# Optimization experiments

Measured on AMD Instinct MI355X. Metric: run time of the kernel, lower is better.

The kernel has to match this reference:

```python
import math
import jax, jax.numpy as jnp
import numpy as np

B, S, H = 4, 2048, 1024

def setup_inputs() -> dict:
    key = jax.random.key(0)
    k1, k2, k3, k4 = jax.random.split(key, 4)
    X = jax.random.normal(k1, (B, S, H), dtype=jnp.float32)
    attention_mask = jax.random.randint(k2, (B, S), 0, 2).astype(jnp.bool_)
    W = jax.random.normal(k3, (H, 3 * H), dtype=jnp.float32) * (1.0 / math.sqrt(H))
    b = jax.random.normal(k4, (3 * H,), dtype=jnp.float32) * 0.02
    return {"X": X, "attention_mask": attention_mask, "W": W, "b": b}

def reference(X, attention_mask, W, b):
    hidden_dim = X.shape[-1]
    # fused QKV projection: (B,S,3H)
    QKV = X @ W + b
    Q, K, V = jnp.split(QKV, 3, axis=-1)
    # scores: (B, S, S)
    scores = jnp.einsum('bqd,bkd->bqk', Q, K) / math.sqrt(hidden_dim)
    # 2D key-padding mask (B,S) -> broadcast over query dim; True = masked
    mask = attention_mask[:, None, :]  # (B,1,S) broadcasts to (B,S,S)
    scores = jnp.where(mask, -jnp.inf, scores)
    attn = jax.nn.softmax(scores, axis=-1)
    # dropout_rate = 0.0 (eval): identity
    return jnp.einsum('bqk,bkd->bqd', attn, V)
```

## Files before the change

### kernel.cpp

```cpp
#include <hip/hip_runtime.h>
#include <hip/hip_bf16.h>
#include <stdint.h>


typedef __attribute__((ext_vector_type(8))) short bf16x8;
typedef __attribute__((ext_vector_type(4))) float f32x4;

__device__ __forceinline__ void async_cp16(const void* g, void* l) {
  __builtin_amdgcn_global_load_lds(
      (const __attribute__((address_space(1))) void*)g,
      (__attribute__((address_space(3))) void*)l, 16, 0, 0);
}

__device__ __forceinline__ uint32_t laddr(const void* p) {
  return (uint32_t)(uintptr_t)(const __attribute__((address_space(3))) void*)p;
}

#define FENCE() asm volatile("" ::: "memory")
#define BAR()                           \
  do {                                  \
    FENCE();                            \
    __builtin_amdgcn_s_barrier();       \
    FENCE();                            \
  } while (0)
#define VMW(N) asm volatile("s_waitcnt vmcnt(" #N ")" ::: "memory")
#define LGKM0()                                            \
  do {                                                     \
    asm volatile("s_waitcnt lgkmcnt(0)" ::: "memory");     \
    __builtin_amdgcn_sched_barrier(0);                     \
  } while (0)
#define DSR(dst, a, OFF) \
  asm volatile("ds_read_b128 %0, %1 offset:" #OFF : "=v"(dst) : "v"(a))

__global__ __launch_bounds__(256) void prep(
    const float* __restrict__ X, __hip_bfloat16* __restrict__ Xb,
    const float* __restrict__ W, __hip_bfloat16* __restrict__ Wt,
    const int* __restrict__ mask, int* __restrict__ idx,
    int* __restrict__ cnt, int* __restrict__ cnt_pad,
    float* __restrict__ rowsum) {
  const int b = blockIdx.x;
  const int tid = threadIdx.x;
  if (b < 8192) {
    int i = (b * 256 + tid) * 4;
    float4 f = *(const float4*)(X + i);
    __hip_bfloat16 o[4];
    o[0] = __float2bfloat16(f.x);
    o[1] = __float2bfloat16(f.y);
    o[2] = __float2bfloat16(f.z);
    o[3] = __float2bfloat16(f.w);
    *(ushort4*)(Xb + i) = *(const ushort4*)o;
    return;
  }
  if (b < 11264) {
    __shared__ float tile[32][33];
    const int t = b - 8192;
    const int bx = (t % 96) * 32;
    const int by = (t / 96) * 32;
    const int tx = tid & 31, ty = tid >> 5;
#pragma unroll
    for (int j = 0; j < 4; ++j)
      tile[ty + j * 8][tx] = W[(int64_t)(by + ty + j * 8) * 3072 + bx + tx];
    __syncthreads();
#pragma unroll
    for (int j = 0; j < 4; ++j)
      Wt[(int64_t)(bx + ty + j * 8) * 1024 + by + tx] =
          __float2bfloat16(tile[tx][ty + j * 8]);
    return;
  }
  {
    const int z = b - 11264;
    const int* mz = mask + z * 2048;
    int* iz = idx + z * 2048;
    const int lane = tid & 63, wave = tid >> 6;
    float* rs = rowsum + z * 2048;
#pragma unroll
    for (int j = 0; j < 8; ++j) rs[tid + j * 256] = 0.f;

    int keep[8];
    int local = 0;
#pragma unroll
    for (int j = 0; j < 8; ++j) {
      keep[j] = (mz[tid * 8 + j] == 0);
      local += keep[j];
    }
    int pre = local;
#pragma unroll
    for (int off = 1; off <= 32; off <<= 1) {
      int n = __shfl_up(pre, off, 64);
      if (lane >= off) pre += n;
    }
    __shared__ int wsum[4];
    if (lane == 63) wsum[wave] = pre;
    __syncthreads();
    int base = 0;
    for (int w = 0; w < wave; ++w) base += wsum[w];
    int excl = base + pre - local;
#pragma unroll
    for (int j = 0; j < 8; ++j)
      if (keep[j]) iz[excl++] = tid * 8 + j;
    if (tid == 255) {
      int tot = base + pre;
      cnt[z] = tot;
      cnt_pad[z] = (tot + 127) & ~127;
    }
  }
}

__global__ __launch_bounds__(256) void gemm_qkv(
    const __hip_bfloat16* __restrict__ Xb, const __hip_bfloat16* __restrict__ Wt,
    const float* __restrict__ bias, const int* __restrict__ idx,
    const int* __restrict__ cnt, const int* __restrict__ cnt_pad,
    __hip_bfloat16* __restrict__ Q, __hip_bfloat16* __restrict__ Kc,
    __hip_bfloat16* __restrict__ Vt) {
  const int z = blockIdx.z;
  const int f = blockIdx.x;
  const int xcd = f & 7, loc = f >> 3;
  const int m0 = ((loc & 7) * 2 + (xcd >> 2)) * 128;
  const int n_idx = (loc >> 3) * 4 + (xcd & 3);
  const bool isQ = (n_idx < 8);
  if (!isQ && m0 >= cnt_pad[z]) return;
  const int n0 = (isQ ? n_idx : n_idx - 8) * 128;
  const __hip_bfloat16* A = Xb + (int64_t)z * 2048 * 1024;
  const __hip_bfloat16* Bt = Wt + (isQ ? 0 : (int64_t)1024 * 1024);
  const float* bv = bias + (isQ ? 0 : 1024);

  const int tid = threadIdx.x;
  const int wave = tid >> 6, lane = tid & 63;
  const int quad = lane >> 4, tr = lane & 15, t7 = tr & 7;
  const int wm = wave & 1, wn = wave >> 1;

  __shared__ __hip_bfloat16 ls[32768];

  const __hip_bfloat16* gsrc[8];
  int loff[8];
  {
    const int srow = lane >> 3;
    const int kcs = (((lane & 7) ^ srow) * 8);
    const int cz = isQ ? 0 : cnt[z];
    const int* idxz = idx + z * 2048;
#pragma unroll
    for (int cc = 0; cc < 8; ++cc) {
      int c = wave * 8 + cc;
      int isA = (c < 16);
      int cr = isA ? c : (c - 16);
      int row = cr * 8 + srow;
      if (isA) {
        int ar = m0 + row;
        if (!isQ) ar = (ar < cz) ? idxz[ar] : 0;
        gsrc[cc] = A + (int64_t)ar * 1024 + kcs;
      } else {
        gsrc[cc] = Bt + (int64_t)(n0 + row) * 1024 + kcs;
      }
      loff[cc] = (isA ? 0 : 8192) + cr * 512;
    }
  }

  uint32_t aAd[2][2], bBd[2][2];
  {
    uint32_t base = laddr(ls);
#pragma unroll
    for (int b = 0; b < 2; ++b)
#pragma unroll
      for (int w = 0; w < 2; ++w) {
        uint32_t col = (uint32_t)(((((w << 2) | quad)) ^ t7) * 16);
        aAd[b][w] = base + b * 32768 + (wm * 64 + tr) * 128 + col;
        bBd[b][w] = base + b * 32768 + 16384 + (wn * 64 + tr) * 128 + col;
      }
  }

  f32x4 acc[4][4];
#pragma unroll
  for (int mi = 0; mi < 4; ++mi)
#pragma unroll
    for (int ni = 0; ni < 4; ++ni) acc[mi][ni] = (f32x4){0.f, 0.f, 0.f, 0.f};

  bf16x8 af[4], bf[4];

#define STAGE(BUF, k0)                                            \
  do {                                                            \
    _Pragma("unroll") for (int cc = 0; cc < 8; ++cc)              \
        async_cp16(gsrc[cc] + (k0), ls + (BUF)*16384 + loff[cc]); \
  } while (0)
#define COMP(BUF)                                                             \
  do {                                                                        \
    _Pragma("unroll") for (int w = 0; w < 2; ++w) {                           \
      DSR(af[0], aAd[BUF][w], 0);                                             \
      DSR(af[1], aAd[BUF][w], 2048);                                          \
      DSR(af[2], aAd[BUF][w], 4096);                                          \
      DSR(af[3], aAd[BUF][w], 6144);                                          \
      DSR(bf[0], bBd[BUF][w], 0);                                             \
      DSR(bf[1], bBd[BUF][w], 2048);                                          \
      DSR(bf[2], bBd[BUF][w], 4096);                                          \
      DSR(bf[3], bBd[BUF][w], 6144);                                          \
      LGKM0();                                                                \
      _Pragma("unroll") for (int mi = 0; mi < 4; ++mi)                        \
          _Pragma("unroll") for (int ni = 0; ni < 4; ++ni) acc[mi][ni] =      \
              __builtin_amdgcn_mfma_f32_16x16x32_bf16(af[mi], bf[ni],         \
                                                      acc[mi][ni], 0, 0, 0);  \
    }                                                                         \
  } while (0)

  STAGE(0, 0);
  for (int it = 0; it < 8; ++it) {
    STAGE(1, (2 * it + 1) * 64);
    VMW(8); BAR();
    COMP(0);
    BAR();
    if (it < 7) {
      STAGE(0, (2 * it + 2) * 64);
      VMW(8);
    } else {
      VMW(0);
    }
    BAR();
    COMP(1);
    BAR();
  }
#undef STAGE
#undef COMP

  const int rowbase = m0 + wm * 64;
  const int colbase = n0 + wn * 64;
  if (isQ) {
    __hip_bfloat16* C = Q + (int64_t)z * 2048 * 1024;
#pragma unroll
    for (int ni = 0; ni < 4; ++ni) {
      int col = colbase + ni * 16 + tr;
      float bb = bv[col];
#pragma unroll
      for (int mi = 0; mi < 4; ++mi) {
        int row = rowbase + mi * 16 + quad * 4;
#pragma unroll
        for (int r = 0; r < 4; ++r)
          C[(int64_t)(row + r) * 1024 + col] =
              __float2bfloat16(acc[mi][ni][r] + bb);
      }
    }
  } else if (n0 < 1024) {
    __hip_bfloat16* C = Kc + (int64_t)z * 2048 * 1024;
#pragma unroll
    for (int ni = 0; ni < 4; ++ni) {
      int col = colbase + ni * 16 + tr;
      float bb = bv[col];
#pragma unroll
      for (int mi = 0; mi < 4; ++mi) {
        int row = rowbase + mi * 16 + quad * 4;
#pragma unroll
        for (int r = 0; r < 4; ++r)
          C[(int64_t)(row + r) * 1024 + col] =
              __float2bfloat16(acc[mi][ni][r] + bb);
      }
    }
  } else {
    __syncthreads();
#pragma unroll
    for (int ni = 0; ni < 4; ++ni) {
      int cl = wn * 64 + ni * 16 + tr;
      float bb = bv[colbase + ni * 16 + tr];
#pragma unroll
      for (int mi = 0; mi < 4; ++mi) {
        int rl = wm * 64 + mi * 16 + quad * 4;
        __hip_bfloat16 h[4];
#pragma unroll
        for (int r = 0; r < 4; ++r) h[r] = __float2bfloat16(acc[mi][ni][r] + bb);
        *(ushort4*)(ls + cl * 136 + rl) = *(const ushort4*)h;
      }
    }
    __syncthreads();
    __hip_bfloat16* Vz = Vt + (int64_t)z * 1024 * 2048;
    const int d0 = n0 - 1024;
    const int seg = tid & 15;
#pragma unroll
    for (int p = 0; p < 8; ++p) {
      int d = p * 16 + (tid >> 4);
      bf16x8 v = *(const bf16x8*)(ls + d * 136 + seg * 8);
      *(bf16x8*)(Vz + (int64_t)(d0 + d) * 2048 + m0 + seg * 8) = v;
    }
  }
}

__global__ __launch_bounds__(256) void gemm_scores(
    const __hip_bfloat16* __restrict__ Qb, const __hip_bfloat16* __restrict__ Kc,
    __hip_bfloat16* __restrict__ Sc, float* __restrict__ rowsum,
    const int* __restrict__ cnt, const int* __restrict__ cnt_pad,
    float scale2) {
  const int z = blockIdx.z;
  const int f = blockIdx.x;
  const int xcd = f & 7, loc = f >> 3;
  const int m0 = ((loc & 7) * 2 + (xcd >> 2)) * 128;
  const int n0 = ((loc >> 3) * 4 + (xcd & 3)) * 128;
  if (n0 >= cnt_pad[z]) return;
  const __hip_bfloat16* A = Qb + (int64_t)z * 2048 * 1024;
  const __hip_bfloat16* Bt = Kc + (int64_t)z * 2048 * 1024;

  const int tid = threadIdx.x;
  const int wave = tid >> 6, lane = tid & 63;
  const int quad = lane >> 4, tr = lane & 15, t7 = tr & 7;
  const int wm = wave & 1, wn = wave >> 1;

  __shared__ __hip_bfloat16 ls[32768];

  const __hip_bfloat16* gsrc[8];
  int loff[8];
  {
    const int srow = lane >> 3;
    const int kcs = (((lane & 7) ^ srow) * 8);
#pragma unroll
    for (int cc = 0; cc < 8; ++cc) {
      int c = wave * 8 + cc;
      int isA = (c < 16);
      int cr = isA ? c : (c - 16);
      int row = cr * 8 + srow;
      gsrc[cc] = isA ? (A + (int64_t)(m0 + row) * 1024 + kcs)
                     : (Bt + (int64_t)(n0 + row) * 1024 + kcs);
      loff[cc] = (isA ? 0 : 8192) + cr * 512;
    }
  }

  uint32_t aAd[2][2], bBd[2][2];
  {
    uint32_t base = laddr(ls);
#pragma unroll
    for (int b = 0; b < 2; ++b)
#pragma unroll
      for (int w = 0; w < 2; ++w) {
        uint32_t col = (uint32_t)(((((w << 2) | quad)) ^ t7) * 16);
        aAd[b][w] = base + b * 32768 + (wm * 64 + tr) * 128 + col;
        bBd[b][w] = base + b * 32768 + 16384 + (wn * 64 + tr) * 128 + col;
      }
  }

  f32x4 acc[4][4];
#pragma unroll
  for (int mi = 0; mi < 4; ++mi)
#pragma unroll
    for (int ni = 0; ni < 4; ++ni) acc[mi][ni] = (f32x4){0.f, 0.f, 0.f, 0.f};

  bf16x8 af[4], bf[4];

#define STAGE(BUF, k0)                                            \
  do {                                                            \
    _Pragma("unroll") for (int cc = 0; cc < 8; ++cc)              \
        async_cp16(gsrc[cc] + (k0), ls + (BUF)*16384 + loff[cc]); \
  } while (0)
#define COMP(BUF)                                                             \
  do {                                                                        \
    _Pragma("unroll") for (int w = 0; w < 2; ++w) {                           \
      DSR(af[0], aAd[BUF][w], 0);                                             \
      DSR(af[1], aAd[BUF][w], 2048);                                          \
      DSR(af[2], aAd[BUF][w], 4096);                                          \
      DSR(af[3], aAd[BUF][w], 6144);                                          \
      DSR(bf[0], bBd[BUF][w], 0);                                             \
      DSR(bf[1], bBd[BUF][w], 2048);                                          \
      DSR(bf[2], bBd[BUF][w], 4096);                                          \
      DSR(bf[3], bBd[BUF][w], 6144);                                          \
      LGKM0();                                                                \
      _Pragma("unroll") for (int mi = 0; mi < 4; ++mi)                        \
          _Pragma("unroll") for (int ni = 0; ni < 4; ++ni) acc[mi][ni] =      \
              __builtin_amdgcn_mfma_f32_16x16x32_bf16(af[mi], bf[ni],         \
                                                      acc[mi][ni], 0, 0, 0);  \
    }                                                                         \
  } while (0)

  STAGE(0, 0);
  for (int it = 0; it < 8; ++it) {
    STAGE(1, (2 * it + 1) * 64);
    VMW(8); BAR();
    COMP(0);
    BAR();
    if (it < 7) {
      STAGE(0, (2 * it + 2) * 64);
      VMW(8);
    } else {
      VMW(0);
    }
    BAR();
    COMP(1);
    BAR();
  }
#undef STAGE
#undef COMP

  const int rowbase = m0 + wm * 64;
  const int colbase = n0 + wn * 64;
  const int cn = cnt[z];
  __hip_bfloat16* C = Sc + (int64_t)z * 2048 * 2048;

  float psum[4][4];
#pragma unroll
  for (int mi = 0; mi < 4; ++mi)
#pragma unroll
    for (int r = 0; r < 4; ++r) psum[mi][r] = 0.f;

#pragma unroll
  for (int ni = 0; ni < 4; ++ni) {
    int col = colbase + ni * 16 + tr;
    bool valid = (col < cn);
#pragma unroll
    for (int mi = 0; mi < 4; ++mi) {
      int row = rowbase + mi * 16 + quad * 4;
#pragma unroll
      for (int r = 0; r < 4; ++r) {
        float e = valid ? exp2f(acc[mi][ni][r] * scale2) : 0.f;
        C[(int64_t)(row + r) * 2048 + col] = __float2bfloat16(e);
        psum[mi][r] += e;
      }
    }
  }
#pragma unroll
  for (int off = 1; off <= 8; off <<= 1)
#pragma unroll
    for (int mi = 0; mi < 4; ++mi)
#pragma unroll
      for (int r = 0; r < 4; ++r)
        psum[mi][r] += __shfl_xor(psum[mi][r], off, 64);
  if (tr == 0) {
    float* rs = rowsum + z * 2048 + rowbase;
#pragma unroll
    for (int mi = 0; mi < 4; ++mi)
#pragma unroll
      for (int r = 0; r < 4; ++r)
        atomicAdd(&rs[mi * 16 + quad * 4 + r], psum[mi][r]);
  }
}

__global__ __launch_bounds__(256) void gemm_pv(
    const __hip_bfloat16* __restrict__ Sc, const __hip_bfloat16* __restrict__ Vt,
    float* __restrict__ out, const float* __restrict__ rowsum,
    const int* __restrict__ cnt_pad) {
  const int z = blockIdx.z;
  const int f = blockIdx.x;
  const int xcd = f & 7, loc = f >> 3;
  const int m0 = ((loc & 7) * 2 + (xcd >> 2)) * 128;
  const int n0 = ((loc >> 3) * 4 + (xcd & 3)) * 128;
  const int Ks = cnt_pad[z];
  const __hip_bfloat16* A = Sc + (int64_t)z * 2048 * 2048;
  const __hip_bfloat16* Bt = Vt + (int64_t)z * 1024 * 2048;

  const int tid = threadIdx.x;
  const int wave = tid >> 6, lane = tid & 63;
  const int quad = lane >> 4, tr = lane & 15, t7 = tr & 7;
  const int wm = wave & 1, wn = wave >> 1;

  __shared__ __hip_bfloat16 ls[32768];

  const __hip_bfloat16* gsrc[8];
  int loff[8];
  {
    const int srow = lane >> 3;
    const int kcs = (((lane & 7) ^ srow) * 8);
#pragma unroll
    for (int cc = 0; cc < 8; ++cc) {
      int c = wave * 8 + cc;
      int isA = (c < 16);
      int cr = isA ? c : (c - 16);
      int row = cr * 8 + srow;
      gsrc[cc] = isA ? (A + (int64_t)(m0 + row) * 2048 + kcs)
                     : (Bt + (int64_t)(n0 + row) * 2048 + kcs);
      loff[cc] = (isA ? 0 : 8192) + cr * 512;
    }
  }

  uint32_t aAd[2][2], bBd[2][2];
  {
    uint32_t base = laddr(ls);
#pragma unroll
    for (int b = 0; b < 2; ++b)
#pragma unroll
      for (int w = 0; w < 2; ++w) {
        uint32_t col = (uint32_t)(((((w << 2) | quad)) ^ t7) * 16);
        aAd[b][w] = base + b * 32768 + (wm * 64 + tr) * 128 + col;
        bBd[b][w] = base + b * 32768 + 16384 + (wn * 64 + tr) * 128 + col;
      }
  }

  f32x4 acc[4][4];
#pragma unroll
  for (int mi = 0; mi < 4; ++mi)
#pragma unroll
    for (int ni = 0; ni < 4; ++ni) acc[mi][ni] = (f32x4){0.f, 0.f, 0.f, 0.f};

  bf16x8 af[4], bf[4];

#define STAGE(BUF, k0)                                            \
  do {                                                            \
    _Pragma("unroll") for (int cc = 0; cc < 8; ++cc)              \
        async_cp16(gsrc[cc] + (k0), ls + (BUF)*16384 + loff[cc]); \
  } while (0)
#define COMP(BUF)                                                             \
  do {                                                                        \
    _Pragma("unroll") for (int w = 0; w < 2; ++w) {                           \
      DSR(af[0], aAd[BUF][w], 0);                                             \
      DSR(af[1], aAd[BUF][w], 2048);                                          \
      DSR(af[2], aAd[BUF][w], 4096);                                          \
      DSR(af[3], aAd[BUF][w], 6144);                                          \
      DSR(bf[0], bBd[BUF][w], 0);                                             \
      DSR(bf[1], bBd[BUF][w], 2048);                                          \
      DSR(bf[2], bBd[BUF][w], 4096);                                          \
      DSR(bf[3], bBd[BUF][w], 6144);                                          \
      LGKM0();                                                                \
      _Pragma("unroll") for (int mi = 0; mi < 4; ++mi)                        \
          _Pragma("unroll") for (int ni = 0; ni < 4; ++ni) acc[mi][ni] =      \
              __builtin_amdgcn_mfma_f32_16x16x32_bf16(af[mi], bf[ni],         \
                                                      acc[mi][ni], 0, 0, 0);  \
    }                                                                         \
  } while (0)

  const int NP = Ks >> 7;
  STAGE(0, 0);
  for (int it = 0; it < NP; ++it) {
    STAGE(1, (2 * it + 1) * 64);
    VMW(8); BAR();
    COMP(0);
    BAR();
    if (it + 1 < NP) {
      STAGE(0, (2 * it + 2) * 64);
      VMW(8);
    } else {
      VMW(0);
    }
    BAR();
    COMP(1);
    BAR();
  }
#undef STAGE
#undef COMP

  const int rowbase = m0 + wm * 64;
  const int colbase = n0 + wn * 64;
  const float* rs = rowsum + z * 2048 + rowbase;
  float invv[4][4];
#pragma unroll
  for (int mi = 0; mi < 4; ++mi)
#pragma unroll
    for (int r = 0; r < 4; ++r) invv[mi][r] = 1.0f / rs[mi * 16 + quad * 4 + r];

  float* C = out + (int64_t)z * 2048 * 1024;
#pragma unroll
  for (int ni = 0; ni < 4; ++ni) {
    int col = colbase + ni * 16 + tr;
#pragma unroll
    for (int mi = 0; mi < 4; ++mi) {
      int row = rowbase + mi * 16 + quad * 4;
#pragma unroll
      for (int r = 0; r < 4; ++r)
        C[(int64_t)(row + r) * 1024 + col] = acc[mi][ni][r] * invv[mi][r];
    }
  }
}

extern "C" void kernel_launch(void* const* d_in, const int* in_sizes, int n_in,
                              void* d_out, int out_size, void* d_ws,
                              size_t ws_size, hipStream_t stream) {
  const float* X = (const float*)d_in[0];
  const int* mask = (const int*)d_in[1];
  const float* W = (const float*)d_in[2];
  const float* bias = (const float*)d_in[3];
  float* out = (float*)d_out;

  char* ws = (char*)d_ws;
  auto alloc = [&](size_t bytes) {
    char* p = ws;
    ws += (bytes + 255) & ~(size_t)255;
    return p;
  };
  __hip_bfloat16* Xb = (__hip_bfloat16*)alloc(8192ULL * 1024 * 2);
  __hip_bfloat16* Wt = (__hip_bfloat16*)alloc(3072ULL * 1024 * 2);
  __hip_bfloat16* Q = (__hip_bfloat16*)alloc(8192ULL * 1024 * 2);
  __hip_bfloat16* Kc = (__hip_bfloat16*)alloc(4ULL * 2048 * 1024 * 2);
  __hip_bfloat16* Vt = (__hip_bfloat16*)alloc(4ULL * 1024 * 2048 * 2);
  __hip_bfloat16* Sc = (__hip_bfloat16*)alloc(4ULL * 2048 * 2048 * 2);
  float* rowsum = (float*)alloc(8192ULL * 4);
  int* idx = (int*)alloc(4ULL * 2048 * 4);
  int* cnt = (int*)alloc(64);
  int* cnt_pad = (int*)alloc(64);

  prep<<<11268, 256, 0, stream>>>(X, Xb, W, Wt, mask, idx, cnt, cnt_pad,
                                  rowsum);
  gemm_qkv<<<dim3(384, 1, 4), 256, 0, stream>>>(Xb, Wt, bias, idx, cnt,
                                                cnt_pad, Q, Kc, Vt);
  gemm_scores<<<dim3(256, 1, 4), 256, 0, stream>>>(
      Q, Kc, Sc, rowsum, cnt, cnt_pad, 0.03125f * 1.4426950408889634f);
  gemm_pv<<<dim3(128, 1, 4), 256, 0, stream>>>(Sc, Vt, out, rowsum, cnt_pad);
}
```

Before: 191.7 us.

## Fuse QKV, scores and PV GEMMs into one persistent kernel with dependency counters

Replaces three separate GEMM launches with a single persistent kernel of 512 blocks. Blocks pull tiles from an atomic work queue, and later stages spin-wait on per-tile completion counters instead of relying on kernel boundaries. The goal is to remove launch gaps and the tail idling at each stage boundary, so that scores and PV tiles can start while earlier stages finish. In exchange it adds atomic polling, extra fences, and the risk of deadlock or stalls if dependency ordering or occupancy assumptions fail.

```diff
diff --git a/kernel.cpp b/kernel.cpp
--- a/kernel.cpp
+++ b/kernel.cpp
@@ -31,150 +31,6 @@
   } while (0)
 #define DSR(dst, a, OFF) \
   asm volatile("ds_read_b128 %0, %1 offset:" #OFF : "=v"(dst) : "v"(a))
-
-__global__ __launch_bounds__(256) void prep(
-    const float* __restrict__ X, __hip_bfloat16* __restrict__ Xb,
-    const float* __restrict__ W, __hip_bfloat16* __restrict__ Wt,
-    const int* __restrict__ mask, int* __restrict__ idx,
-    int* __restrict__ cnt, int* __restrict__ cnt_pad,
-    float* __restrict__ rowsum) {
-  const int b = blockIdx.x;
-  const int tid = threadIdx.x;
-  if (b < 8192) {
-    int i = (b * 256 + tid) * 4;
-    float4 f = *(const float4*)(X + i);
-    __hip_bfloat16 o[4];
-    o[0] = __float2bfloat16(f.x);
-    o[1] = __float2bfloat16(f.y);
-    o[2] = __float2bfloat16(f.z);
-    o[3] = __float2bfloat16(f.w);
-    *(ushort4*)(Xb + i) = *(const ushort4*)o;
-    return;
-  }
-  if (b < 11264) {
-    __shared__ float tile[32][33];
-    const int t = b - 8192;
-    const int bx = (t % 96) * 32;
-    const int by = (t / 96) * 32;
-    const int tx = tid & 31, ty = tid >> 5;
-#pragma unroll
-    for (int j = 0; j < 4; ++j)
-      tile[ty + j * 8][tx] = W[(int64_t)(by + ty + j * 8) * 3072 + bx + tx];
-    __syncthreads();
-#pragma unroll
-    for (int j = 0; j < 4; ++j)
-      Wt[(int64_t)(bx + ty + j * 8) * 1024 + by + tx] =
-          __float2bfloat16(tile[tx][ty + j * 8]);
-    return;
-  }
-  {
-    const int z = b - 11264;
-    const int* mz = mask + z * 2048;
-    int* iz = idx + z * 2048;
-    const int lane = tid & 63, wave = tid >> 6;
-    float* rs = rowsum + z * 2048;
-#pragma unroll
-    for (int j = 0; j < 8; ++j) rs[tid + j * 256] = 0.f;
-
-    int keep[8];
-    int local = 0;
-#pragma unroll
-    for (int j = 0; j < 8; ++j) {
-      keep[j] = (mz[tid * 8 + j] == 0);
-      local += keep[j];
-    }
-    int pre = local;
-#pragma unroll
-    for (int off = 1; off <= 32; off <<= 1) {
-      int n = __shfl_up(pre, off, 64);
-      if (lane >= off) pre += n;
-    }
-    __shared__ int wsum[4];
-    if (lane == 63) wsum[wave] = pre;
-    __syncthreads();
-    int base = 0;
-    for (int w = 0; w < wave; ++w) base += wsum[w];
-    int excl = base + pre - local;
-#pragma unroll
-    for (int j = 0; j < 8; ++j)
-      if (keep[j]) iz[excl++] = tid * 8 + j;
-    if (tid == 255) {
-      int tot = base + pre;
-      cnt[z] = tot;
-      cnt_pad[z] = (tot + 127) & ~127;
-    }
-  }
-}
-
-__global__ __launch_bounds__(256) void gemm_qkv(
-    const __hip_bfloat16* __restrict__ Xb, const __hip_bfloat16* __restrict__ Wt,
-    const float* __restrict__ bias, const int* __restrict__ idx,
-    const int* __restrict__ cnt, const int* __restrict__ cnt_pad,
-    __hip_bfloat16* __restrict__ Q, __hip_bfloat16* __restrict__ Kc,
-    __hip_bfloat16* __restrict__ Vt) {
-  const int z = blockIdx.z;
-  const int f = blockIdx.x;
-  const int xcd = f & 7, loc = f >> 3;
-  const int m0 = ((loc & 7) * 2 + (xcd >> 2)) * 128;
-  const int n_idx = (loc >> 3) * 4 + (xcd & 3);
-  const bool isQ = (n_idx < 8);
-  if (!isQ && m0 >= cnt_pad[z]) return;
-  const int n0 = (isQ ? n_idx : n_idx - 8) * 128;
-  const __hip_bfloat16* A = Xb + (int64_t)z * 2048 * 1024;
-  const __hip_bfloat16* Bt = Wt + (isQ ? 0 : (int64_t)1024 * 1024);
-  const float* bv = bias + (isQ ? 0 : 1024);
-
-  const int tid = threadIdx.x;
-  const int wave = tid >> 6, lane = tid & 63;
-  const int quad = lane >> 4, tr = lane & 15, t7 = tr & 7;
-  const int wm = wave & 1, wn = wave >> 1;
-
-  __shared__ __hip_bfloat16 ls[32768];
-
-  const __hip_bfloat16* gsrc[8];
-  int loff[8];
-  {
-    const int srow = lane >> 3;
-    const int kcs = (((lane & 7) ^ srow) * 8);
-    const int cz = isQ ? 0 : cnt[z];
-    const int* idxz = idx + z * 2048;
-#pragma unroll
-    for (int cc = 0; cc < 8; ++cc) {
-      int c = wave * 8 + cc;
-      int isA = (c < 16);
-      int cr = isA ? c : (c - 16);
-      int row = cr * 8 + srow;
-      if (isA) {
-        int ar = m0 + row;
-        if (!isQ) ar = (ar < cz) ? idxz[ar] : 0;
-        gsrc[cc] = A + (int64_t)ar * 1024 + kcs;
-      } else {
-        gsrc[cc] = Bt + (int64_t)(n0 + row) * 1024 + kcs;
-      }
-      loff[cc] = (isA ? 0 : 8192) + cr * 512;
-    }
-  }
-
-  uint32_t aAd[2][2], bBd[2][2];
-  {
-    uint32_t base = laddr(ls);
-#pragma unroll
-    for (int b = 0; b < 2; ++b)
-#pragma unroll
-      for (int w = 0; w < 2; ++w) {
-        uint32_t col = (uint32_t)(((((w << 2) | quad)) ^ t7) * 16);
-        aAd[b][w] = base + b * 32768 + (wm * 64 + tr) * 128 + col;
-        bBd[b][w] = base + b * 32768 + 16384 + (wn * 64 + tr) * 128 + col;
-      }
-  }
-
-  f32x4 acc[4][4];
-#pragma unroll
-  for (int mi = 0; mi < 4; ++mi)
-#pragma unroll
-    for (int ni = 0; ni < 4; ++ni) acc[mi][ni] = (f32x4){0.f, 0.f, 0.f, 0.f};
-
-  bf16x8 af[4], bf[4];
 
 #define STAGE(BUF, k0)                                            \
   do {                                                            \
@@ -200,122 +56,103 @@
     }                                                                         \
   } while (0)
 
-  STAGE(0, 0);
-  for (int it = 0; it < 8; ++it) {
-    STAGE(1, (2 * it + 1) * 64);
-    VMW(8); BAR();
-    COMP(0);
-    BAR();
-    if (it < 7) {
-      STAGE(0, (2 * it + 2) * 64);
-      VMW(8);
-    } else {
-      VMW(0);
+__device__ __forceinline__ void wait_ge(int* p, int target) {
+  while (__hip_atomic_load(p, __ATOMIC_RELAXED, __HIP_MEMORY_SCOPE_AGENT) <
+         target)
+    __builtin_amdgcn_s_sleep(4);
+}
+
+__global__ __launch_bounds__(256) void prep(
+    const float* __restrict__ X, __hip_bfloat16* __restrict__ Xb,
+    const float* __restrict__ W, __hip_bfloat16* __restrict__ Wt,
+    const int* __restrict__ mask, int* __restrict__ idx,
+    int* __restrict__ cnt, int* __restrict__ cnt_pad,
+    float* __restrict__ rowsum, int* __restrict__ gsync) {
+  const int b = blockIdx.x;
+  const int tid = threadIdx.x;
+  if (b < 8192) {
+    int i = (b * 256 + tid) * 4;
+    float4 f = *(const float4*)(X + i);
+    __hip_bfloat16 o[4];
+    o[0] = __float2bfloat16(f.x);
+    o[1] = __float2bfloat16(f.y);
+    o[2] = __float2bfloat16(f.z);
+    o[3] = __float2bfloat16(f.w);
+    *(ushort4*)(Xb + i) = *(const ushort4*)o;
+    return;
+  }
+  if (b < 11264) {
+    __shared__ float tile[32][33];
+    const int t = b - 8192;
+    const int bx = (t % 96) * 32;
+    const int by = (t / 96) * 32;
+    const int tx = tid & 31, ty = tid >> 5;
+#pragma unroll
+    for (int j = 0; j < 4; ++j)
+      tile[ty + j * 8][tx] = W[(int64_t)(by + ty + j * 8) * 3072 + bx + tx];
+    __syncthreads();
+#pragma unroll
+    for (int j = 0; j < 4; ++j)
+      Wt[(int64_t)(bx + ty + j * 8) * 1024 + by + tx] =
+          __float2bfloat16(tile[tx][ty + j * 8]);
+    return;
+  }
+  if (b < 11268) {
+    const int z = b - 11264;
+    const int* mz = mask + z * 2048;
+    int* iz = idx + z * 2048;
+    const int lane = tid & 63, wave = tid >> 6;
+    float* rs = rowsum + z * 2048;
+#pragma unroll
+    for (int j = 0; j < 8; ++j) rs[tid + j * 256] = 0.f;
+
+    int keep[8];
+    int local = 0;
+#pragma unroll
+    for (int j = 0; j < 8; ++j) {
+      keep[j] = (mz[tid * 8 + j] == 0);
+      local += keep[j];
     }
-    BAR();
-    COMP(1);
-    BAR();
+    int pre = local;
+#pragma unroll
+    for (int off = 1; off <= 32; off <<= 1) {
+      int n = __shfl_up(pre, off, 64);
+      if (lane >= off) pre += n;
+    }
+    __shared__ int wsum[4];
+    if (lane == 63) wsum[wave] = pre;
+    __syncthreads();
+    int base = 0;
+    for (int w = 0; w < wave; ++w) base += wsum[w];
+    int excl = base + pre - local;
+#pragma unroll
+    for (int j = 0; j < 8; ++j)
+      if (keep[j]) iz[excl++] = tid * 8 + j;
+    if (tid == 255) {
+      int tot = base + pre;
+      cnt[z] = tot;
+      cnt_pad[z] = (tot + 127) & ~127;
+    }
+    return;
   }
-#undef STAGE
-#undef COMP
-
-  const int rowbase = m0 + wm * 64;
-  const int colbase = n0 + wn * 64;
-  if (isQ) {
-    __hip_bfloat16* C = Q + (int64_t)z * 2048 * 1024;
-#pragma unroll
-    for (int ni = 0; ni < 4; ++ni) {
-      int col = colbase + ni * 16 + tr;
-      float bb = bv[col];
-#pragma unroll
-      for (int mi = 0; mi < 4; ++mi) {
-        int row = rowbase + mi * 16 + quad * 4;
-#pragma unroll
-        for (int r = 0; r < 4; ++r)
-          C[(int64_t)(row + r) * 1024 + col] =
-              __float2bfloat16(acc[mi][ni][r] + bb);
-      }
-    }
-  } else if (n0 < 1024) {
-    __hip_bfloat16* C = Kc + (int64_t)z * 2048 * 1024;
-#pragma unroll
-    for (int ni = 0; ni < 4; ++ni) {
-      int col = colbase + ni * 16 + tr;
-      float bb = bv[col];
-#pragma unroll
-      for (int mi = 0; mi < 4; ++mi) {
-        int row = rowbase + mi * 16 + quad * 4;
-#pragma unroll
-        for (int r = 0; r < 4; ++r)
-          C[(int64_t)(row + r) * 1024 + col] =
-              __float2bfloat16(acc[mi][ni][r] + bb);
-      }
-    }
-  } else {
-    __syncthreads();
-#pragma unroll
-    for (int ni = 0; ni < 4; ++ni) {
-      int cl = wn * 64 + ni * 16 + tr;
-      float bb = bv[colbase + ni * 16 + tr];
-#pragma unroll
-      for (int mi = 0; mi < 4; ++mi) {
-        int rl = wm * 64 + mi * 16 + quad * 4;
-        __hip_bfloat16 h[4];
-#pragma unroll
-        for (int r = 0; r < 4; ++r) h[r] = __float2bfloat16(acc[mi][ni][r] + bb);
-        *(ushort4*)(ls + cl * 136 + rl) = *(const ushort4*)h;
-      }
-    }
-    __syncthreads();
-    __hip_bfloat16* Vz = Vt + (int64_t)z * 1024 * 2048;
-    const int d0 = n0 - 1024;
-    const int seg = tid & 15;
-#pragma unroll
-    for (int p = 0; p < 8; ++p) {
-      int d = p * 16 + (tid >> 4);
-      bf16x8 v = *(const bf16x8*)(ls + d * 136 + seg * 8);
-      *(bf16x8*)(Vz + (int64_t)(d0 + d) * 2048 + m0 + seg * 8) = v;
-    }
-  }
+  gsync[tid] = 0;
 }
 
-__global__ __launch_bounds__(256) void gemm_scores(
-    const __hip_bfloat16* __restrict__ Qb, const __hip_bfloat16* __restrict__ Kc,
-    __hip_bfloat16* __restrict__ Sc, float* __restrict__ rowsum,
+__global__ __launch_bounds__(256) void fused(
+    const __hip_bfloat16* __restrict__ Xb, const __hip_bfloat16* __restrict__ Wt,
+    const float* __restrict__ bias, const int* __restrict__ idx,
     const int* __restrict__ cnt, const int* __restrict__ cnt_pad,
-    float scale2) {
-  const int z = blockIdx.z;
-  const int f = blockIdx.x;
-  const int xcd = f & 7, loc = f >> 3;
-  const int m0 = ((loc & 7) * 2 + (xcd >> 2)) * 128;
-  const int n0 = ((loc >> 3) * 4 + (xcd & 3)) * 128;
-  if (n0 >= cnt_pad[z]) return;
-  const __hip_bfloat16* A = Qb + (int64_t)z * 2048 * 1024;
-  const __hip_bfloat16* Bt = Kc + (int64_t)z * 2048 * 1024;
-
+    __hip_bfloat16* __restrict__ Q, __hip_bfloat16* __restrict__ Kc,
+    __hip_bfloat16* __restrict__ Vt, __hip_bfloat16* __restrict__ Sc,
+    float* __restrict__ rowsum, float* __restrict__ out, float scale2,
+    int* __restrict__ gsync) {
+  __shared__ __hip_bfloat16 ls[32768];
   const int tid = threadIdx.x;
   const int wave = tid >> 6, lane = tid & 63;
   const int quad = lane >> 4, tr = lane & 15, t7 = tr & 7;
   const int wm = wave & 1, wn = wave >> 1;
-
-  __shared__ __hip_bfloat16 ls[32768];
-
-  const __hip_bfloat16* gsrc[8];
-  int loff[8];
-  {
-    const int srow = lane >> 3;
-    const int kcs = (((lane & 7) ^ srow) * 8);
-#pragma unroll
-    for (int cc = 0; cc < 8; ++cc) {
-      int c = wave * 8 + cc;
-      int isA = (c < 16);
-      int cr = isA ? c : (c - 16);
-      int row = cr * 8 + srow;
-      gsrc[cc] = isA ? (A + (int64_t)(m0 + row) * 1024 + kcs)
-                     : (Bt + (int64_t)(n0 + row) * 1024 + kcs);
-      loff[cc] = (isA ? 0 : 8192) + cr * 512;
-    }
-  }
+  const int srow = lane >> 3;
+  const int kcs = ((lane & 7) ^ srow) * 8;
 
   uint32_t aAd[2][2], bBd[2][2];
   {
@@ -330,221 +167,328 @@
       }
   }
 
-  f32x4 acc[4][4];
-#pragma unroll
-  for (int mi = 0; mi < 4; ++mi)
-#pragma unroll
-    for (int ni = 0; ni < 4; ++ni) acc[mi][ni] = (f32x4){0.f, 0.f, 0.f, 0.f};
-
-  bf16x8 af[4], bf[4];
-
-#define STAGE(BUF, k0)                                            \
-  do {                                                            \
-    _Pragma("unroll") for (int cc = 0; cc < 8; ++cc)              \
-        async_cp16(gsrc[cc] + (k0), ls + (BUF)*16384 + loff[cc]); \
-  } while (0)
-#define COMP(BUF)                                                             \
-  do {                                                                        \
-    _Pragma("unroll") for (int w = 0; w < 2; ++w) {                           \
-      DSR(af[0], aAd[BUF][w], 0);                                             \
-      DSR(af[1], aAd[BUF][w], 2048);                                          \
-      DSR(af[2], aAd[BUF][w], 4096);                                          \
-      DSR(af[3], aAd[BUF][w], 6144);                                          \
-      DSR(bf[0], bBd[BUF][w], 0);                                             \
-      DSR(bf[1], bBd[BUF][w], 2048);                                          \
-      DSR(bf[2], bBd[BUF][w], 4096);                                          \
-      DSR(bf[3], bBd[BUF][w], 6144);                                          \
-      LGKM0();                                                                \
-      _Pragma("unroll") for (int mi = 0; mi < 4; ++mi)                        \
-          _Pragma("unroll") for (int ni = 0; ni < 4; ++ni) acc[mi][ni] =      \
-              __builtin_amdgcn_mfma_f32_16x16x32_bf16(af[mi], bf[ni],         \
-                                                      acc[mi][ni], 0, 0, 0);  \
-    }                                                                         \
-  } while (0)
-
-  STAGE(0, 0);
-  for (int it = 0; it < 8; ++it) {
-    STAGE(1, (2 * it + 1) * 64);
-    VMW(8); BAR();
-    COMP(0);
-    BAR();
-    if (it < 7) {
-      STAGE(0, (2 * it + 2) * 64);
-      VMW(8);
+  for (;;) {
+    __syncthreads();
+    if (tid == 0) {
+      int tt = __hip_atomic_fetch_add(&gsync[0], 1, __ATOMIC_RELAXED,
+                                      __HIP_MEMORY_SCOPE_AGENT);
+      *(int*)ls = tt;
+    }
+    __syncthreads();
+    const int t = *(const int*)ls;
+    __syncthreads();
+    if (t >= 3072) break;
+
+    if (t < 1536) {
+      const int z = t / 384, f = t % 384;
+      const int xcd = f & 7, loc = f >> 3;
+      const int m0 = ((loc & 7) * 2 + (xcd >> 2)) * 128;
+      const int n_idx = (loc >> 3) * 4 + (xcd & 3);
+      const bool isQ = (n_idx < 8);
+      if (!isQ && m0 >= cnt_pad[z]) continue;
+      const int n0 = (isQ ? n_idx : n_idx - 8) * 128;
+      const __hip_bfloat16* A = Xb + (int64_t)z * 2048 * 1024;
+      const __hip_bfloat16* Bt = Wt + (isQ ? 0 : (int64_t)1024 * 1024);
+      const float* bv = bias + (isQ ? 0 : 1024);
+
+      const __hip_bfloat16* gsrc[8];
+      int loff[8];
+      {
+        const int cz = isQ ? 0 : cnt[z];
+        const int* idxz = idx + z * 2048;
+#pragma unroll
+        for (int cc = 0; cc < 8; ++cc) {
+          int c = wave * 8 + cc;
+          int isA = (c < 16);
+          int cr = isA ? c : (c - 16);
+          int row = cr * 8 + srow;
+          if (isA) {
+            int ar = m0 + row;
+            if (!isQ) ar = (ar < cz) ? idxz[ar] : 0;
+            gsrc[cc] = A + (int64_t)ar * 1024 + kcs;
+          } else {
+            gsrc[cc] = Bt + (int64_t)(n0 + row) * 1024 + kcs;
+          }
+          loff[cc] = (isA ? 0 : 8192) + cr * 512;
+        }
+      }
+
+      f32x4 acc[4][4];
+#pragma unroll
+      for (int mi = 0; mi < 4; ++mi)
+#pragma unroll
+        for (int ni = 0; ni < 4; ++ni)
+          acc[mi][ni] = (f32x4){0.f, 0.f, 0.f, 0.f};
+      bf16x8 af[4], bf[4];
+
+      STAGE(0, 0);
+      for (int it = 0; it < 8; ++it) {
+        STAGE(1, (2 * it + 1) * 64);
+        VMW(8); BAR();
+        COMP(0);
+        BAR();
+        if (it < 7) {
+          STAGE(0, (2 * it + 2) * 64);
+          VMW(8);
+        } else {
+          VMW(0);
+        }
+        BAR();
+        COMP(1);
+        BAR();
+      }
+
+      const int rowbase = m0 + wm * 64;
+      const int colbase = n0 + wn * 64;
+      if (isQ) {
+        __hip_bfloat16* C = Q + (int64_t)z * 2048 * 1024;
+#pragma unroll
+        for (int ni = 0; ni < 4; ++ni) {
+          int col = colbase + ni * 16 + tr;
+          float bb = bv[col];
+#pragma unroll
+          for (int mi = 0; mi < 4; ++mi) {
+            int row = rowbase + mi * 16 + quad * 4;
+#pragma unroll
+            for (int r = 0; r < 4; ++r)
+              C[(int64_t)(row + r) * 1024 + col] =
+                  __float2bfloat16(acc[mi][ni][r] + bb);
+          }
+        }
+      } else if (n0 < 1024) {
+        __hip_bfloat16* C = Kc + (int64_t)z * 2048 * 1024;
+#pragma unroll
+        for (int ni = 0; ni < 4; ++ni) {
+          int col = colbase + ni * 16 + tr;
+          float bb = bv[col];
+#pragma unroll
+          for (int mi = 0; mi < 4; ++mi) {
+            int row = rowbase + mi * 16 + quad * 4;
+#pragma unroll
+            for (int r = 0; r < 4; ++r)
+              C[(int64_t)(row + r) * 1024 + col] =
+                  __float2bfloat16(acc[mi][ni][r] + bb);
+          }
+        }
+      } else {
+        __syncthreads();
+#pragma unroll
+        for (int ni = 0; ni < 4; ++ni) {
+          int cl = wn * 64 + ni * 16 + tr;
+          float bb = bv[colbase + ni * 16 + tr];
+#pragma unroll
+          for (int mi = 0; mi < 4; ++mi) {
+            int rl = wm * 64 + mi * 16 + quad * 4;
+            __hip_bfloat16 h[4];
+#pragma unroll
+            for (int r = 0; r < 4; ++r)
+              h[r] = __float2bfloat16(acc[mi][ni][r] + bb);
+            *(ushort4*)(ls + cl * 136 + rl) = *(const ushort4*)h;
+          }
+        }
+        __syncthreads();
+        __hip_bfloat16* Vz = Vt + (int64_t)z * 1024 * 2048;
+        const int d0 = n0 - 1024;
+        const int seg = tid & 15;
+#pragma unroll
+        for (int p = 0; p < 8; ++p) {
+          int d = p * 16 + (tid >> 4);
+          bf16x8 v = *(const bf16x8*)(ls + d * 136 + seg * 8);
+          *(bf16x8*)(Vz + (int64_t)(d0 + d) * 2048 + m0 + seg * 8) = v;
+        }
+      }
+      __threadfence();
+      __syncthreads();
+      if (tid == 0) {
+        int* p = isQ ? &gsync[1 + z * 16 + (m0 >> 7)]
+                     : (n0 < 1024 ? &gsync[65 + z * 16 + (m0 >> 7)]
+                                  : &gsync[129 + z * 8 + ((n0 - 1024) >> 7)]);
+        __hip_atomic_fetch_add(p, 1, __ATOMIC_RELEASE,
+                               __HIP_MEMORY_SCOPE_AGENT);
+      }
+    } else if (t < 2560) {
+      const int t2 = t - 1536;
+      const int z = t2 >> 8, f = t2 & 255;
+      const int xcd = f & 7, loc = f >> 3;
+      const int m0 = ((loc & 7) * 2 + (xcd >> 2)) * 128;
+      const int n0 = ((loc >> 3) * 4 + (xcd & 3)) * 128;
+      if (n0 >= cnt_pad[z]) continue;
+      if (tid == 0) {
+        wait_ge(&gsync[1 + z * 16 + (m0 >> 7)], 8);
+        wait_ge(&gsync[65 + z * 16 + (n0 >> 7)], 8);
+      }
+      __syncthreads();
+      __threadfence();
+
+      const __hip_bfloat16* A = Q + (int64_t)z * 2048 * 1024;
+      const __hip_bfloat16* Bt = Kc + (int64_t)z * 2048 * 1024;
+
+      const __hip_bfloat16* gsrc[8];
+      int loff[8];
+      {
+#pragma unroll
+        for (int cc = 0; cc < 8; ++cc) {
+          int c = wave * 8 + cc;
+          int isA = (c < 16);
+          int cr = isA ? c : (c - 16);
+          int row = cr * 8 + srow;
+          gsrc[cc] = isA ? (A + (int64_t)(m0 + row) * 1024 + kcs)
+                         : (Bt + (int64_t)(n0 + row) * 1024 + kcs);
+          loff[cc] = (isA ? 0 : 8192) + cr * 512;
+        }
+      }
+
+      f32x4 acc[4][4];
+#pragma unroll
+      for (int mi = 0; mi < 4; ++mi)
+#pragma unroll
+        for (int ni = 0; ni < 4; ++ni)
+          acc[mi][ni] = (f32x4){0.f, 0.f, 0.f, 0.f};
+      bf16x8 af[4], bf[4];
+
+      STAGE(0, 0);
+      for (int it = 0; it < 8; ++it) {
+        STAGE(1, (2 * it + 1) * 64);
+        VMW(8); BAR();
+        COMP(0);
+        BAR();
+        if (it < 7) {
+          STAGE(0, (2 * it + 2) * 64);
+          VMW(8);
+        } else {
+          VMW(0);
+        }
+        BAR();
+        COMP(1);
+        BAR();
+      }
+
+      const int rowbase = m0 + wm * 64;
+      const int colbase = n0 + wn * 64;
+      const int cn = cnt[z];
+      __hip_bfloat16* C = Sc + (int64_t)z * 2048 * 2048;
+
+      float psum[4][4];
+#pragma unroll
+      for (int mi = 0; mi < 4; ++mi)
+#pragma unroll
+        for (int r = 0; r < 4; ++r) psum[mi][r] = 0.f;
+
+#pragma unroll
+      for (int ni = 0; ni < 4; ++ni) {
+        int col = colbase + ni * 16 + tr;
+        bool valid = (col < cn);
+#pragma unroll
+        for (int mi = 0; mi < 4; ++mi) {
+          int row = rowbase + mi * 16 + quad * 4;
+#pragma unroll
+          for (int r = 0; r < 4; ++r) {
+            float e = valid ? exp2f(acc[mi][ni][r] * scale2) : 0.f;
+            C[(int64_t)(row + r) * 2048 + col] = __float2bfloat16(e);
+            psum[mi][r] += e;
+          }
+        }
+      }
+#pragma unroll
+      for (int off = 1; off <= 8; off <<= 1)
+#pragma unroll
+        for (int mi = 0; mi < 4; ++mi)
+#pragma unroll
+          for (int r = 0; r < 4; ++r)
+            psum[mi][r] += __shfl_xor(psum[mi][r], off, 64);
+      if (tr == 0) {
+        float* rs = rowsum + z * 2048 + rowbase;
+#pragma unroll
+        for (int mi = 0; mi < 4; ++mi)
+#pragma unroll
+          for (int r = 0; r < 4; ++r)
+            atomicAdd(&rs[mi * 16 + quad * 4 + r], psum[mi][r]);
+      }
+      __threadfence();
+      __syncthreads();
+      if (tid == 0)
+        __hip_atomic_fetch_add(&gsync[161 + z * 16 + (m0 >> 7)], 1,
+                               __ATOMIC_RELEASE, __HIP_MEMORY_SCOPE_AGENT);
     } else {
-      VMW(0);
-    }
-    BAR();
-    COMP(1);
-    BAR();
-  }
-#undef STAGE
-#undef COMP
-
-  const int rowbase = m0 + wm * 64;
-  const int colbase = n0 + wn * 64;
-  const int cn = cnt[z];
-  __hip_bfloat16* C = Sc + (int64_t)z * 2048 * 2048;
-
-  float psum[4][4];
-#pragma unroll
-  for (int mi = 0; mi < 4; ++mi)
-#pragma unroll
-    for (int r = 0; r < 4; ++r) psum[mi][r] = 0.f;
-
-#pragma unroll
-  for (int ni = 0; ni < 4; ++ni) {
-    int col = colbase + ni * 16 + tr;
-    bool valid = (col < cn);
-#pragma unroll
-    for (int mi = 0; mi < 4; ++mi) {
-      int row = rowbase + mi * 16 + quad * 4;
-#pragma unroll
-      for (int r = 0; r < 4; ++r) {
-        float e = valid ? exp2f(acc[mi][ni][r] * scale2) : 0.f;
-        C[(int64_t)(row + r) * 2048 + col] = __float2bfloat16(e);
-        psum[mi][r] += e;
-      }
-    }
-  }
-#pragma unroll
-  for (int off = 1; off <= 8; off <<= 1)
-#pragma unroll
-    for (int mi = 0; mi < 4; ++mi)
-#pragma unroll
-      for (int r = 0; r < 4; ++r)
-        psum[mi][r] += __shfl_xor(psum[mi][r], off, 64);
-  if (tr == 0) {
-    float* rs = rowsum + z * 2048 + rowbase;
-#pragma unroll
-    for (int mi = 0; mi < 4; ++mi)
-#pragma unroll
-      for (int r = 0; r < 4; ++r)
-        atomicAdd(&rs[mi * 16 + quad * 4 + r], psum[mi][r]);
-  }
-}
-
-__global__ __launch_bounds__(256) void gemm_pv(
-    const __hip_bfloat16* __restrict__ Sc, const __hip_bfloat16* __restrict__ Vt,
-    float* __restrict__ out, const float* __restrict__ rowsum,
-    const int* __restrict__ cnt_pad) {
-  const int z = blockIdx.z;
-  const int f = blockIdx.x;
-  const int xcd = f & 7, loc = f >> 3;
-  const int m0 = ((loc & 7) * 2 + (xcd >> 2)) * 128;
-  const int n0 = ((loc >> 3) * 4 + (xcd & 3)) * 128;
-  const int Ks = cnt_pad[z];
-  const __hip_bfloat16* A = Sc + (int64_t)z * 2048 * 2048;
-  const __hip_bfloat16* Bt = Vt + (int64_t)z * 1024 * 2048;
-
-  const int tid = threadIdx.x;
-  const int wave = tid >> 6, lane = tid & 63;
-  const int quad = lane >> 4, tr = lane & 15, t7 = tr & 7;
-  const int wm = wave & 1, wn = wave >> 1;
-
-  __shared__ __hip_bfloat16 ls[32768];
-
-  const __hip_bfloat16* gsrc[8];
-  int loff[8];
-  {
-    const int srow = lane >> 3;
-    const int kcs = (((lane & 7) ^ srow) * 8);
-#pragma unroll
-    for (int cc = 0; cc < 8; ++cc) {
-      int c = wave * 8 + cc;
-      int isA = (c < 16);
-      int cr = isA ? c : (c - 16);
-      int row = cr * 8 + srow;
-      gsrc[cc] = isA ? (A + (int64_t)(m0 + row) * 2048 + kcs)
-                     : (Bt + (int64_t)(n0 + row) * 2048 + kcs);
-      loff[cc] = (isA ? 0 : 8192) + cr * 512;
-    }
-  }
-
-  uint32_t aAd[2][2], bBd[2][2];
-  {
-    uint32_t base = laddr(ls);
-#pragma unroll
-    for (int b = 0; b < 2; ++b)
-#pragma unroll
-      for (int w = 0; w < 2; ++w) {
-        uint32_t col = (uint32_t)(((((w << 2) | quad)) ^ t7) * 16);
-        aAd[b][w] = base + b * 32768 + (wm * 64 + tr) * 128 + col;
-        bBd[b][w] = base + b * 32768 + 16384 + (wn * 64 + tr) * 128 + col;
-      }
-  }
-
-  f32x4 acc[4][4];
-#pragma unroll
-  for (int mi = 0; mi < 4; ++mi)
-#pragma unroll
-    for (int ni = 0; ni < 4; ++ni) acc[mi][ni] = (f32x4){0.f, 0.f, 0.f, 0.f};
-
-  bf16x8 af[4], bf[4];
-
-#define STAGE(BUF, k0)                                            \
-  do {                                                            \
-    _Pragma("unroll") for (int cc = 0; cc < 8; ++cc)              \
-        async_cp16(gsrc[cc] + (k0), ls + (BUF)*16384 + loff[cc]); \
-  } while (0)
-#define COMP(BUF)                                                             \
-  do {                                                                        \
-    _Pragma("unroll") for (int w = 0; w < 2; ++w) {                           \
-      DSR(af[0], aAd[BUF][w], 0);                                             \
-      DSR(af[1], aAd[BUF][w], 2048);                                          \
-      DSR(af[2], aAd[BUF][w], 4096);                                          \
-      DSR(af[3], aAd[BUF][w], 6144);                                          \
-      DSR(bf[0], bBd[BUF][w], 0);                                             \
-      DSR(bf[1], bBd[BUF][w], 2048);                                          \
-      DSR(bf[2], bBd[BUF][w], 4096);                                          \
-      DSR(bf[3], bBd[BUF][w], 6144);                                          \
-      LGKM0();                                                                \
-      _Pragma("unroll") for (int mi = 0; mi < 4; ++mi)                        \
-          _Pragma("unroll") for (int ni = 0; ni < 4; ++ni) acc[mi][ni] =      \
-              __builtin_amdgcn_mfma_f32_16x16x32_bf16(af[mi], bf[ni],         \
-                                                      acc[mi][ni], 0, 0, 0);  \
-    }                                                                         \
-  } while (0)
-
-  const int NP = Ks >> 7;
-  STAGE(0, 0);
-  for (int it = 0; it < NP; ++it) {
-    STAGE(1, (2 * it + 1) * 64);
-    VMW(8); BAR();
-    COMP(0);
-    BAR();
-    if (it + 1 < NP) {
-      STAGE(0, (2 * it + 2) * 64);
-      VMW(8);
-    } else {
-      VMW(0);
-    }
-    BAR();
-    COMP(1);
-    BAR();
-  }
-#undef STAGE
-#undef COMP
-
-  const int rowbase = m0 + wm * 64;
-  const int colbase = n0 + wn * 64;
-  const float* rs = rowsum + z * 2048 + rowbase;
-  float invv[4][4];
-#pragma unroll
-  for (int mi = 0; mi < 4; ++mi)
-#pragma unroll
-    for (int r = 0; r < 4; ++r) invv[mi][r] = 1.0f / rs[mi * 16 + quad * 4 + r];
-
-  float* C = out + (int64_t)z * 2048 * 1024;
-#pragma unroll
-  for (int ni = 0; ni < 4; ++ni) {
-    int col = colbase + ni * 16 + tr;
-#pragma unroll
-    for (int mi = 0; mi < 4; ++mi) {
-      int row = rowbase + mi * 16 + quad * 4;
-#pragma unroll
-      for (int r = 0; r < 4; ++r)
-        C[(int64_t)(row + r) * 1024 + col] = acc[mi][ni][r] * invv[mi][r];
+      const int t3 = t - 2560;
+      const int z = t3 >> 7, f = t3 & 127;
+      const int xcd = f & 7, loc = f >> 3;
+      const int m0 = ((loc & 7) * 2 + (xcd >> 2)) * 128;
+      const int n0 = ((loc >> 3) * 4 + (xcd & 3)) * 128;
+      const int Ks = cnt_pad[z];
+      const int np = Ks >> 7;
+      if (tid == 0) {
+        wait_ge(&gsync[161 + z * 16 + (m0 >> 7)], np);
+        wait_ge(&gsync[129 + z * 8 + (n0 >> 7)], np);
+      }
+      __syncthreads();
+      __threadfence();
+
+      const __hip_bfloat16* A = Sc + (int64_t)z * 2048 * 2048;
+      const __hip_bfloat16* Bt = Vt + (int64_t)z * 1024 * 2048;
+
+      const __hip_bfloat16* gsrc[8];
+      int loff[8];
+      {
+#pragma unroll
+        for (int cc = 0; cc < 8; ++cc) {
+          int c = wave * 8 + cc;
+          int isA = (c < 16);
+          int cr = isA ? c : (c - 16);
+          int row = cr * 8 + srow;
+          gsrc[cc] = isA ? (A + (int64_t)(m0 + row) * 2048 + kcs)
+                         : (Bt + (int64_t)(n0 + row) * 2048 + kcs);
+          loff[cc] = (isA ? 0 : 8192) + cr * 512;
+        }
+      }
+
+      f32x4 acc[4][4];
+#pragma unroll
+      for (int mi = 0; mi < 4; ++mi)
+#pragma unroll
+        for (int ni = 0; ni < 4; ++ni)
+          acc[mi][ni] = (f32x4){0.f, 0.f, 0.f, 0.f};
+      bf16x8 af[4], bf[4];
+
+      STAGE(0, 0);
+      for (int it = 0; it < np; ++it) {
+        STAGE(1, (2 * it + 1) * 64);
+        VMW(8); BAR();
+        COMP(0);
+        BAR();
+        if (it + 1 < np) {
+          STAGE(0, (2 * it + 2) * 64);
+          VMW(8);
+        } else {
+          VMW(0);
+        }
+        BAR();
+        COMP(1);
+        BAR();
+      }
+
+      const int rowbase = m0 + wm * 64;
+      const int colbase = n0 + wn * 64;
+      const float* rs = rowsum + z * 2048 + rowbase;
+      float invv[4][4];
+#pragma unroll
+      for (int mi = 0; mi < 4; ++mi)
+#pragma unroll
+        for (int r = 0; r < 4; ++r)
+          invv[mi][r] = 1.0f / rs[mi * 16 + quad * 4 + r];
+
+      float* C = out + (int64_t)z * 2048 * 1024;
+#pragma unroll
+      for (int ni = 0; ni < 4; ++ni) {
+        int col = colbase + ni * 16 + tr;
+#pragma unroll
+        for (int mi = 0; mi < 4; ++mi) {
+          int row = rowbase + mi * 16 + quad * 4;
+#pragma unroll
+          for (int r = 0; r < 4; ++r)
+            C[(int64_t)(row + r) * 1024 + col] = acc[mi][ni][r] * invv[mi][r];
+        }
+      }
     }
   }
 }
@@ -574,12 +518,11 @@
   int* idx = (int*)alloc(4ULL * 2048 * 4);
   int* cnt = (int*)alloc(64);
   int* cnt_pad = (int*)alloc(64);
-
-  prep<<<11268, 256, 0, stream>>>(X, Xb, W, Wt, mask, idx, cnt, cnt_pad,
-                                  rowsum);
-  gemm_qkv<<<dim3(384, 1, 4), 256, 0, stream>>>(Xb, Wt, bias, idx, cnt,
-                                                cnt_pad, Q, Kc, Vt);
-  gemm_scores<<<dim3(256, 1, 4), 256, 0, stream>>>(
-      Q, Kc, Sc, rowsum, cnt, cnt_pad, 0.03125f * 1.4426950408889634f);
-  gemm_pv<<<dim3(128, 1, 4), 256, 0, stream>>>(Sc, Vt, out, rowsum, cnt_pad);
+  int* gsync = (int*)alloc(256 * 4);
+
+  prep<<<11269, 256, 0, stream>>>(X, Xb, W, Wt, mask, idx, cnt, cnt_pad,
+                                  rowsum, gsync);
+  fused<<<512, 256, 0, stream>>>(Xb, Wt, bias, idx, cnt, cnt_pad, Q, Kc, Vt,
+                                 Sc, rowsum, out,
+                                 0.03125f * 1.4426950408889634f, gsync);
 }
```

Result: slower. 589.2 us (+207.4%).
